# Optimization experiments

Hardware: AMD Instinct MI355X
Metric: run time of the kernel (lower is better)

## Reference

```python
import jax, jax.numpy as jnp
import numpy as np

LN_EPS = 1e-5


def _layer_norm(h, g, b):
    mu = jnp.mean(h, axis=-1, keepdims=True)
    var = jnp.mean((h - mu) ** 2, axis=-1, keepdims=True)
    return (h - mu) / jnp.sqrt(var + LN_EPS) * g + b


def setup_inputs() -> dict:
    key = jax.random.key(0)
    ks = jax.random.split(key, 12)
    B, N, D = 2, 2048, 768
    H, Dh = 12, 64
    Dp = D // 4  # 192, DynamicPositionBias width
    s = lambda fan_in: 1.0 / np.sqrt(fan_in)
    return {
        "x": jax.random.normal(ks[0], (B, N, D), jnp.float32),
        "qkv_w": jax.random.normal(ks[1], (D, 3 * H * Dh), jnp.float32) * s(D),
        "qkv_b": jax.random.normal(ks[2], (3 * H * Dh,), jnp.float32) * 0.02,
        "out_w": jax.random.normal(ks[3], (H * Dh, D), jnp.float32) * s(H * Dh),
        "out_b": jax.random.normal(ks[4], (D,), jnp.float32) * 0.02,
        "dpb_w_in": jax.random.normal(ks[5], (1, Dp), jnp.float32),
        "dpb_b_in": jax.random.normal(ks[6], (Dp,), jnp.float32) * 0.02,
        "dpb_w_hid": jax.random.normal(ks[7], (3, Dp, Dp), jnp.float32) * s(Dp),
        "dpb_b_hid": jax.random.normal(ks[8], (3, Dp), jnp.float32) * 0.02,
        "dpb_ln_g": jnp.ones((4, Dp), jnp.float32),
        "dpb_ln_b": jnp.zeros((4, Dp), jnp.float32),
        "dpb_w_out": jax.random.normal(ks[9], (Dp, 12), jnp.float32) * s(Dp),
        "dpb_b_out": jax.random.normal(ks[10], (12,), jnp.float32) * 0.02,
    }


def _dpb_bias(n, w_in, b_in, w_hid, b_hid, ln_g, ln_b, w_out, b_out):
    # positions -n+1 .. n-1, log-distance transform
    pos = jnp.arange(-n + 1, n, dtype=jnp.float32)[:, None]  # [2n-1, 1]
    pos = jnp.sign(pos) * jnp.log(jnp.abs(pos) + 1.0)
    h = jax.nn.silu(_layer_norm(pos @ w_in + b_in, ln_g[0], ln_b[0]))
    for l in range(3):
        h = jax.nn.silu(_layer_norm(h @ w_hid[l] + b_hid[l], ln_g[l + 1], ln_b[l + 1]))
    vals = h @ w_out + b_out  # [2n-1, H]
    idx = jnp.arange(n)[:, None] - jnp.arange(n)[None, :] + (n - 1)  # [n, n]
    bias = vals[idx]  # [n, n, H]
    return jnp.transpose(bias, (2, 0, 1))  # [H, n, n]


def reference(x, qkv_w, qkv_b, out_w, out_b,
              dpb_w_in, dpb_b_in, dpb_w_hid, dpb_b_hid,
              dpb_ln_g, dpb_ln_b, dpb_w_out, dpb_b_out):
    B, N, D = x.shape
    H = dpb_w_out.shape[-1]
    qkv = x @ qkv_w + qkv_b  # [B, N, 3*H*Dh]
    q, k, v = jnp.split(qkv, 3, axis=-1)
    split_heads = lambda t: jnp.transpose(t.reshape(B, N, H, -1), (0, 2, 1, 3))
    q, k, v = split_heads(q), split_heads(k), split_heads(v)  # [B, H, N, Dh]
    Dh = q.shape[-1]

    bias = _dpb_bias(N, dpb_w_in, dpb_b_in, dpb_w_hid, dpb_b_hid,
                     dpb_ln_g, dpb_ln_b, dpb_w_out, dpb_b_out)  # [H, N, N]

    scale = Dh ** -0.5
    sim = jnp.einsum("bhid,bhjd->bhij", q, k) * scale + bias[None]
    attn = jax.nn.softmax(sim, axis=-1)
    o = jnp.einsum("bhij,bhjd->bhid", attn, v)  # [B, H, N, Dh]
    o = jnp.transpose(o, (0, 2, 1, 3)).reshape(B, N, H * Dh)
    return o @ out_w + out_b
```

## Files before the change

kernel.cpp:

```cpp
#include <hip/hip_runtime.h>
#include <stdint.h>
#include <stddef.h>

typedef __bf16 bf16;
typedef __bf16 bf16x8 __attribute__((ext_vector_type(8)));
typedef float floatx4 __attribute__((ext_vector_type(4)));

typedef __attribute__((address_space(1))) void as1_void;
typedef __attribute__((address_space(3))) void as3_void;

__device__ __forceinline__ void async_ld16(const void* g, void* l) {
    __builtin_amdgcn_global_load_lds((as1_void*)g, (as3_void*)l, 16, 0, 0);
}

__device__ __forceinline__ floatx4 mfma16(bf16x8 a, bf16x8 b, floatx4 c) {
    return __builtin_amdgcn_mfma_f32_16x16x32_bf16(a, b, c, 0, 0, 0);
}

__device__ __forceinline__ unsigned cvtpk_bf16(float lo, float hi) {
    unsigned r;
    asm("v_cvt_pk_bf16_f32 %0, %1, %2" : "=v"(r) : "v"(lo), "v"(hi));
    return r;
}
__device__ __forceinline__ void pl32swap(unsigned &a, unsigned &b) {
    asm("v_permlane32_swap_b32 %0, %1" : "+v"(a), "+v"(b));
}
__device__ __forceinline__ void pl16swap(unsigned &a, unsigned &b) {
    asm("v_permlane16_swap_b32 %0, %1" : "+v"(a), "+v"(b));
}

#define LOG2E 1.4426950408889634f
#define SM_M2 24.0f
#define DP 192

__device__ __forceinline__ float ldsc(const void* p, size_t i, int isbf) {
    return isbf ? (float)((const bf16*)p)[i] : ((const float*)p)[i];
}
__device__ __forceinline__ bf16x8 ld8(const void* p, size_t i, int isbf) {
    if (isbf) return *(const bf16x8*)((const bf16*)p + i);
    const float* f = (const float*)p + i;
    float4 lo = *(const float4*)(f);
    float4 hi = *(const float4*)(f + 4);
    bf16x8 r;
    r[0]=(bf16)lo.x; r[1]=(bf16)lo.y; r[2]=(bf16)lo.z; r[3]=(bf16)lo.w;
    r[4]=(bf16)hi.x; r[5]=(bf16)hi.y; r[6]=(bf16)hi.z; r[7]=(bf16)hi.w;
    return r;
}
__device__ __forceinline__ int get_fl(const uint32_t* lng) {
    return (lng[0] == 0x3F803F80u) ? 1 : 0;
}

__device__ void transpose_body(const void* in, bf16* out, int R, int C,
                               int bx, int by, int fl, bf16 (*tile)[65]) {
    int c0 = bx * 64, r0 = by * 64;
    for (int i = threadIdx.x; i < 64*64; i += 256) {
        int rr = i >> 6, cc = i & 63;
        int gr = r0 + rr, gc = c0 + cc;
        tile[rr][cc] = (gr < R && gc < C)
                       ? (bf16)ldsc(in, (size_t)gr * C + gc, fl) : (bf16)0.0f;
    }
    __syncthreads();
    for (int i = threadIdx.x; i < 64*64; i += 256) {
        int rr = i >> 6, cc = i & 63;
        int oR = c0 + rr, oC = r0 + cc;
        if (oR < C && oC < R) out[(size_t)oR * R + oC] = tile[cc][rr];
    }
}

__global__ __launch_bounds__(256) void prep_kernel(
    const void* __restrict__ qkv_w, const void* __restrict__ out_w,
    bf16* __restrict__ wt_qkv, bf16* __restrict__ wt_out,
    const void* __restrict__ w_hid, const void* __restrict__ w_out,
    bf16* __restrict__ WtH, bf16* __restrict__ Wt12,
    const uint32_t* __restrict__ lngw,
    const void* __restrict__ x, bf16* __restrict__ xbf)
{
    __shared__ bf16 tile[64][65];
    const int fl = get_fl(lngw);
    const int bid = blockIdx.x;
    if (bid < 432) {
        transpose_body(qkv_w, wt_qkv, 768, 2304, bid % 36, bid / 36, fl, tile);
        return;
    }
    if (bid < 576) {
        int b2 = bid - 432;
        transpose_body(out_w, wt_out, 768, 768, b2 % 12, b2 / 12, fl, tile);
        return;
    }
    if (bid < 603) {
        int b2 = bid - 576, l = b2 / 9, t9 = b2 % 9;
        transpose_body((const char*)w_hid + (size_t)l * DP * DP * (fl ? 2 : 4),
                       WtH + (size_t)l * DP * DP, DP, DP, t9 % 3, t9 / 3,
                       fl, tile);
        return;
    }
    if (bid < 606) {
        transpose_body(w_out, Wt12, 192, 12, 0, bid - 603, fl, tile);
        return;
    }
    size_t base = (size_t)(bid - 606) * 6144 + threadIdx.x * 8;
    #pragma unroll
    for (int c = 0; c < 3; c++)
        *(bf16x8*)(xbf + base + c*2048) = ld8(x, base + c*2048, fl);
}

#define GK 768
#define HS 200

__global__ __launch_bounds__(256) void gemm0_dpb_kernel(
    const bf16* __restrict__ A, const bf16* __restrict__ Bt,
    const void* __restrict__ bias, const uint32_t* __restrict__ lngw,
    bf16* __restrict__ out0, bf16* __restrict__ out1, bf16* __restrict__ out2,
    const void* __restrict__ w_in, const void* __restrict__ b_in,
    const void* __restrict__ b_hid, const void* __restrict__ ln_g,
    const void* __restrict__ ln_b, const void* __restrict__ b_out,
    const bf16* __restrict__ WtH, const bf16* __restrict__ Wt12,
    float* __restrict__ vals_t)
{
    __shared__ __align__(16) char smem[16896];
    const int fl = get_fl(lngw);
    const int tid = threadIdx.x;
    const int wave = tid >> 6, lane = tid & 63;
    const int g = lane >> 4, cl = lane & 15;

    if (blockIdx.x >= 576) {
        bf16*  Hb   = (bf16*)smem;
        float* redS = (float*)(smem + 6400);
        float* redQ = (float*)(smem + 6656);
        const int pbase = (blockIdx.x - 576) * 16;

        float tpos[4];
        #pragma unroll
        for (int rg = 0; rg < 4; rg++) {
            int p = pbase + g*4 + rg;
            float pv = (float)p - 2047.0f;
            float sg = (pv > 0.0f) ? 1.0f : ((pv < 0.0f) ? -1.0f : 0.0f);
            tpos[rg] = sg * logf(fabsf(pv) + 1.0f);
        }
        int col[3];
        #pragma unroll
        for (int tt = 0; tt < 3; tt++) col[tt] = (wave*3 + tt)*16 + cl;

        floatx4 acc[3];
        #pragma unroll
        for (int tt = 0; tt < 3; tt++) {
            float wi = ldsc(w_in, col[tt], fl), bi = ldsc(b_in, col[tt], fl);
            #pragma unroll
            for (int rg = 0; rg < 4; rg++) acc[tt][rg] = tpos[rg]*wi + bi;
        }

        #pragma unroll 1
        for (int l = 0; l < 4; l++) {
            float s1[4], s2[4];
            #pragma unroll
            for (int rg = 0; rg < 4; rg++) {
                s1[rg] = acc[0][rg] + acc[1][rg] + acc[2][rg];
                s2[rg] = acc[0][rg]*acc[0][rg] + acc[1][rg]*acc[1][rg]
                       + acc[2][rg]*acc[2][rg];
            }
            #pragma unroll
            for (int m = 1; m <= 8; m <<= 1)
                #pragma unroll
                for (int rg = 0; rg < 4; rg++) {
                    s1[rg] += __shfl_xor(s1[rg], m);
                    s2[rg] += __shfl_xor(s2[rg], m);
                }
            if (cl == 0)
                #pragma unroll
                for (int rg = 0; rg < 4; rg++) {
                    redS[wave*16 + g*4 + rg] = s1[rg];
                    redQ[wave*16 + g*4 + rg] = s2[rg];
                }
            __syncthreads();
            float mu[4], rstd[4];
            #pragma unroll
            for (int rg = 0; rg < 4; rg++) {
                int row = g*4 + rg;
                float S = redS[row] + redS[16+row] + redS[32+row] + redS[48+row];
                float Q = redQ[row] + redQ[16+row] + redQ[32+row] + redQ[48+row];
                float m_ = S * (1.0f/DP);
                float v_ = Q * (1.0f/DP) - m_*m_;
                mu[rg] = m_;
                rstd[rg] = 1.0f / sqrtf(v_ + 1e-5f);
            }
            #pragma unroll
            for (int tt = 0; tt < 3; tt++) {
                float ga = ldsc(ln_g, l*DP + col[tt], fl);
                float be = ldsc(ln_b, l*DP + col[tt], fl);
                #pragma unroll
                for (int rg = 0; rg < 4; rg++) {
                    float y = (acc[tt][rg] - mu[rg]) * rstd[rg] * ga + be;
                    float sil = y / (1.0f + __expf(-y));
                    Hb[(g*4 + rg)*HS + col[tt]] = (bf16)sil;
                }
            }
            __syncthreads();
            if (l == 3) break;
            #pragma unroll
            for (int tt = 0; tt < 3; tt++) {
                float bh = ldsc(b_hid, l*DP + col[tt], fl);
                #pragma unroll
                for (int rg = 0; rg < 4; rg++) acc[tt][rg] = bh;
            }
            const bf16* Wl = WtH + (size_t)l * DP * DP;
            #pragma unroll
            for (int ks = 0; ks < 6; ks++) {
                bf16x8 af = *(const bf16x8*)(Hb + cl*HS + ks*32 + g*8);
                #pragma unroll
                for (int tt = 0; tt < 3; tt++) {
                    bf16x8 bfv = *(const bf16x8*)(Wl + (size_t)col[tt]*DP
                                                  + ks*32 + g*8);
                    acc[tt] = mfma16(af, bfv, acc[tt]);
                }
            }
        }
        if (wave == 0) {
            floatx4 facc = {};
            if (cl < 12) {
                float bo = ldsc(b_out, cl, fl);
                #pragma unroll
                for (int rg = 0; rg < 4; rg++) facc[rg] = bo;
            }
            #pragma unroll
            for (int ks = 0; ks < 6; ks++) {
                bf16x8 af = *(const bf16x8*)(Hb + cl*HS + ks*32 + g*8);
                bf16x8 bfv = {};
                if (cl < 12)
                    bfv = *(const bf16x8*)(Wt12 + (size_t)cl*DP + ks*32 + g*8);
                facc = mfma16(af, bfv, facc);
            }
            if (cl < 12)
                #pragma unroll
                for (int rg = 0; rg < 4; rg++) {
                    int p = pbase + g*4 + rg;
                    if (p < 4095) vals_t[cl*4095 + p] = facc[rg];
                }
        }
        return;
    }

    bf16* As = (bf16*)smem;
    bf16* Bs = (bf16*)(smem + 8192);
    const int xcd8 = blockIdx.x & 7, slot = blockIdx.x >> 3;
    const int m0 = (xcd8*4 + slot/18) * 128, n0 = (slot % 18) * 128;
    const int wm = (wave >> 1) * 64, wn = (wave & 1) * 64;

    const int e0 = wave*512 + lane*8;
    const int e1 = e0 + 2048;
    const int r0 = e0 >> 5, c0e = e0 & 31;
    const int r1 = e1 >> 5, c1e = e1 & 31;
    const bf16* Ag0 = A  + (size_t)(m0 + r0) * GK + c0e;
    const bf16* Ag1 = A  + (size_t)(m0 + r1) * GK + c1e;
    const bf16* Bg0 = Bt + (size_t)(n0 + r0) * GK + c0e;
    const bf16* Bg1 = Bt + (size_t)(n0 + r1) * GK + c1e;
    bf16* Al0 = As + e0;
    bf16* Al1 = As + e1;
    bf16* Bl0 = Bs + e0;
    bf16* Bl1 = Bs + e1;

    const int frow = lane & 15, fk = (lane >> 4) * 8;
    floatx4 acc[4][4] = {};

    for (int k0 = 0; k0 < GK; k0 += 32) {
        __syncthreads();
        async_ld16(Ag0 + k0, Al0);
        async_ld16(Ag1 + k0, Al1);
        async_ld16(Bg0 + k0, Bl0);
        async_ld16(Bg1 + k0, Bl1);
        __syncthreads();
        bf16x8 af[4], bfr[4];
        #pragma unroll
        for (int i = 0; i < 4; i++)
            af[i] = *(const bf16x8*)(As + (wm + i*16 + frow)*32 + fk);
        #pragma unroll
        for (int j = 0; j < 4; j++)
            bfr[j] = *(const bf16x8*)(Bs + (wn + j*16 + frow)*32 + fk);
        #pragma unroll
        for (int i = 0; i < 4; i++)
            #pragma unroll
            for (int j = 0; j < 4; j++)
                acc[i][j] = mfma16(af[i], bfr[j], acc[i][j]);
    }

    #pragma unroll
    for (int i = 0; i < 4; i++) {
        #pragma unroll
        for (int j = 0; j < 4; j++) {
            int Cc = n0 + wn + j*16 + cl;
            float bv = ldsc(bias, Cc, fl);
            #pragma unroll
            for (int rg = 0; rg < 4; rg++) {
                int R = m0 + wm + i*16 + g*4 + rg;
                float val = acc[i][j][rg] + bv;
                int which = Cc / 768;
                int c2 = Cc - which * 768;
                int hh = c2 >> 6, dd = c2 & 63;
                int bb = R >> 11, nn = R & 2047;
                if (which == 2) {
                    out2[(((size_t)(bb*12 + hh) * 64 + dd) * 2048) + nn]
                        = (bf16)val;
                } else {
                    bf16* dst = (which == 0) ? out0 : out1;
                    dst[((size_t)(bb*12 + hh) * 2048 + nn) * 64 + dd] = (bf16)val;
                }
            }
        }
    }
}

__global__ __launch_bounds__(256) void gemm_out(
    const bf16* __restrict__ A, const bf16* __restrict__ Bt,
    const void* __restrict__ bias, const uint32_t* __restrict__ lngw,
    void* __restrict__ out0)
{
    __shared__ __align__(16) bf16 As[128*32];
    __shared__ __align__(16) bf16 Bs[128*32];
    const int fl  = get_fl(lngw);
    const int tid = threadIdx.x;
    const int wave = tid >> 6, lane = tid & 63;
    const int m0 = blockIdx.y * 128, n0 = blockIdx.x * 128;
    const int wm = (wave >> 1) * 64, wn = (wave & 1) * 64;

    const int e0 = wave*512 + lane*8;
    const int e1 = e0 + 2048;
    const int r0 = e0 >> 5, c0e = e0 & 31;
    const int r1 = e1 >> 5, c1e = e1 & 31;
    const bf16* Ag0 = A  + (size_t)(m0 + r0) * GK + c0e;
    const bf16* Ag1 = A  + (size_t)(m0 + r1) * GK + c1e;
    const bf16* Bg0 = Bt + (size_t)(n0 + r0) * GK + c0e;
    const bf16* Bg1 = Bt + (size_t)(n0 + r1) * GK + c1e;
    bf16* Al0 = As + e0;
    bf16* Al1 = As + e1;
    bf16* Bl0 = Bs + e0;
    bf16* Bl1 = Bs + e1;

    const int frow = lane & 15, fk = (lane >> 4) * 8;
    floatx4 acc[4][4] = {};

    for (int k0 = 0; k0 < GK; k0 += 32) {
        __syncthreads();
        async_ld16(Ag0 + k0, Al0);
        async_ld16(Ag1 + k0, Al1);
        async_ld16(Bg0 + k0, Bl0);
        async_ld16(Bg1 + k0, Bl1);
        __syncthreads();
        bf16x8 af[4], bfr[4];
        #pragma unroll
        for (int i = 0; i < 4; i++)
            af[i] = *(const bf16x8*)(As + (wm + i*16 + frow)*32 + fk);
        #pragma unroll
        for (int j = 0; j < 4; j++)
            bfr[j] = *(const bf16x8*)(Bs + (wn + j*16 + frow)*32 + fk);
        #pragma unroll
        for (int i = 0; i < 4; i++)
            #pragma unroll
            for (int j = 0; j < 4; j++)
                acc[i][j] = mfma16(af[i], bfr[j], acc[i][j]);
    }

    const int g = lane >> 4, cl = lane & 15;
    #pragma unroll
    for (int i = 0; i < 4; i++) {
        #pragma unroll
        for (int j = 0; j < 4; j++) {
            int Cc = n0 + wn + j*16 + cl;
            float bv = ldsc(bias, Cc, fl);
            #pragma unroll
            for (int rg = 0; rg < 4; rg++) {
                int R = m0 + wm + i*16 + g*4 + rg;
                float val = acc[i][j][rg] + bv;
                size_t oi = (size_t)R * 768 + Cc;
                if (fl) ((bf16*)out0)[oi]  = (bf16)val;
                else    ((float*)out0)[oi] = val;
            }
        }
    }
}

__global__ __launch_bounds__(256) void attn_kernel(
    const bf16* __restrict__ qws, const bf16* __restrict__ kws,
    const bf16* __restrict__ vwst, const float* __restrict__ vals_t,
    bf16* __restrict__ ows)
{
    __shared__ __align__(16) bf16 Qs[64*72];
    __shared__ __align__(16) bf16 Ks[2][64*72];
    __shared__ __align__(16) bf16 Vt[2][64*72];
    __shared__ float bias_s[2][128];

    const int tid = threadIdx.x;
    const int wave = tid >> 6, lane = tid & 63;
    const int g = lane >> 4, cl = lane & 15;
    const int xcd8 = blockIdx.x & 7, slot = blockIdx.x >> 3;
    const int bh_ = xcd8*3 + (slot >> 5);
    const int q0 = (slot & 31) * 64;
    const int h = bh_ % 12, b = bh_ / 12;
    const size_t bh = (size_t)bh_;
    const bf16* qp  = qws  + bh * 2048 * 64;
    const bf16* kp  = kws  + bh * 2048 * 64;
    const bf16* vpt = vwst + bh * 64 * 2048;
    const float* vrow = vals_t + h * 4095;

    for (int i = tid; i < 512; i += 256) {
        int r = i >> 3, c = (i & 7) * 8;
        *(bf16x8*)(Qs + r*72 + c) = *(const bf16x8*)(qp + (size_t)(q0 + r)*64 + c);
    }

    const int sr0 = tid >> 3, sc0 = (tid & 7) * 8;
    const int sr1 = sr0 + 32;

    bf16x8 kreg0 = *(const bf16x8*)(kp + (size_t)sr0 * 64 + sc0);
    bf16x8 kreg1 = *(const bf16x8*)(kp + (size_t)sr1 * 64 + sc0);
    bf16x8 vreg0 = *(const bf16x8*)(vpt + (size_t)sr0 * 2048 + sc0);
    bf16x8 vreg1 = *(const bf16x8*)(vpt + (size_t)sr1 * 2048 + sc0);
    float  breg  = 0.0f;
    if (tid < 127) breg = vrow[q0 + 1984 + tid];
    *(bf16x8*)(Ks[0] + sr0*72 + sc0) = kreg0;
    *(bf16x8*)(Ks[0] + sr1*72 + sc0) = kreg1;
    *(bf16x8*)(Vt[0] + sr0*72 + sc0) = vreg0;
    *(bf16x8*)(Vt[0] + sr1*72 + sc0) = vreg1;
    if (tid < 127) bias_s[0][tid] = breg * LOG2E - SM_M2;

    kreg0 = *(const bf16x8*)(kp + (size_t)(64 + sr0) * 64 + sc0);
    kreg1 = *(const bf16x8*)(kp + (size_t)(64 + sr1) * 64 + sc0);
    vreg0 = *(const bf16x8*)(vpt + (size_t)sr0 * 2048 + 64 + sc0);
    vreg1 = *(const bf16x8*)(vpt + (size_t)sr1 * 2048 + 64 + sc0);
    if (tid < 127) breg = vrow[q0 - 64 + 1984 + tid];

    __syncthreads();
    bf16x8 aq0 = *(const bf16x8*)(Qs + (wave*16 + cl)*72 + g*8);
    bf16x8 aq1 = *(const bf16x8*)(Qs + (wave*16 + cl)*72 + 32 + g*8);

    floatx4 accO[4] = {};
    float lsum = 0.0f;
    const int il_b = wave*16 + g*4;
    const float c1 = 0.125f * LOG2E;
    const int bbase = wave*16 + cl - 4*g + 63;

    for (int j = 0; j < 32; ++j) {
        const int cur = j & 1;
        if (j + 1 < 32) {
            bf16* Kn = Ks[cur ^ 1];
            bf16* Vn = Vt[cur ^ 1];
            *(bf16x8*)(Kn + sr0*72 + sc0) = kreg0;
            *(bf16x8*)(Kn + sr1*72 + sc0) = kreg1;
            *(bf16x8*)(Vn + sr0*72 + sc0) = vreg0;
            *(bf16x8*)(Vn + sr1*72 + sc0) = vreg1;
            if (tid < 127) bias_s[cur ^ 1][tid] = breg * LOG2E - SM_M2;
        }
        if (j + 2 < 32) {
            const int nj = (j + 2) * 64;
            kreg0 = *(const bf16x8*)(kp + (size_t)(nj + sr0) * 64 + sc0);
            kreg1 = *(const bf16x8*)(kp + (size_t)(nj + sr1) * 64 + sc0);
            vreg0 = *(const bf16x8*)(vpt + (size_t)sr0 * 2048 + nj + sc0);
            vreg1 = *(const bf16x8*)(vpt + (size_t)sr1 * 2048 + nj + sc0);
            if (tid < 127) breg = vrow[q0 - nj + 1984 + tid];
        }

        const bf16* Kc = Ks[cur];
        const bf16* Vc = Vt[cur];
        const float* bs = bias_s[cur];

        floatx4 accS[4];
        #pragma unroll
        for (int jt = 0; jt < 4; jt++) {
            bf16x8 ak0 = *(const bf16x8*)(Kc + (jt*16 + cl)*72 + g*8);
            bf16x8 ak1 = *(const bf16x8*)(Kc + (jt*16 + cl)*72 + 32 + g*8);
            floatx4 z = {};
            z = mfma16(ak0, aq0, z);
            z = mfma16(ak1, aq1, z);
            accS[jt] = z;
        }

        unsigned pk[4][2];
        #pragma unroll
        for (int jt = 0; jt < 4; jt++) {
            float pv[4];
            #pragma unroll
            for (int rg = 0; rg < 4; rg++) {
                float x2 = fmaf(accS[jt][rg], c1, bs[bbase - jt*16 - rg]);
                x2 = fminf(x2, 80.0f);
                pv[rg] = __builtin_amdgcn_exp2f(x2);
            }
            lsum += (pv[0] + pv[1]) + (pv[2] + pv[3]);
            pk[jt][0] = cvtpk_bf16(pv[0], pv[1]);
            pk[jt][1] = cvtpk_bf16(pv[2], pv[3]);
        }

        bf16x8 ap[2];
        #pragma unroll
        for (int kst = 0; kst < 2; kst++) {
            unsigned e0p = pk[2*kst][0], f0p = pk[2*kst+1][0];
            unsigned e1p = pk[2*kst][1], f1p = pk[2*kst+1][1];
            pl32swap(e0p, f0p);
            pl16swap(e0p, f0p);
            pl32swap(e1p, f1p);
            pl16swap(e1p, f1p);
            union { unsigned u[4]; bf16x8 v; } uu;
            uu.u[0] = e0p; uu.u[1] = e1p; uu.u[2] = f0p; uu.u[3] = f1p;
            ap[kst] = uu.v;
        }

        #pragma unroll
        for (int dt = 0; dt < 4; dt++) {
            #pragma unroll
            for (int kst = 0; kst < 2; kst++) {
                bf16x8 bv = *(const bf16x8*)(Vc + (dt*16 + cl)*72 + kst*32 + g*8);
                accO[dt] = mfma16(ap[kst], bv, accO[dt]);
            }
        }

        __syncthreads();
    }

    lsum += __shfl_xor(lsum, 16);
    lsum += __shfl_xor(lsum, 32);

    #pragma unroll
    for (int rg = 0; rg < 4; rg++) {
        float l = __shfl(lsum, g*4 + rg);
        float inv = 1.0f / l;
        size_t row = (size_t)(b*2048 + q0 + il_b + rg) * 768 + h*64;
        #pragma unroll
        for (int dt = 0; dt < 4; dt++)
            ows[row + dt*16 + cl] = (bf16)(accO[dt][rg] * inv);
    }
}

extern "C" void kernel_launch(void* const* d_in, const int* in_sizes, int n_in,
                              void* d_out, int out_size, void* d_ws, size_t ws_size,
                              hipStream_t stream)
{
    (void)in_sizes; (void)n_in; (void)out_size;
    const void* x     = d_in[0];
    const void* qkv_w = d_in[1];
    const void* qkv_b = d_in[2];
    const void* out_w = d_in[3];
    const void* out_b = d_in[4];
    const void* w_in  = d_in[5];
    const void* b_in  = d_in[6];
    const void* w_hid = d_in[7];
    const void* b_hid = d_in[8];
    const void* ln_g  = d_in[9];
    const void* ln_b  = d_in[10];
    const void* w_out = d_in[11];
    const void* b_out = d_in[12];

    const size_t NEED = 4915200 + 4ull*6291456;
    if (ws_size < NEED) return;

    char* ws = (char*)d_ws;
    float* vals_t = (float*)(ws);
    bf16*  wt_qkv = (bf16*)(ws + 196608);
    bf16*  wt_out = (bf16*)(ws + 196608 + 3538944);
    bf16*  q_ws   = (bf16*)(ws + 4915200);
    bf16*  k_ws   = (bf16*)(ws + 4915200 + 6291456);
    bf16*  v_wst  = (bf16*)(ws + 4915200 + 2*6291456);
    bf16*  o_ws   = (bf16*)(ws + 4915200 + 3*6291456);
    bf16*  x_bf   = o_ws;
    bf16*  WtH    = (bf16*)d_out;
    bf16*  Wt12   = WtH + 3*DP*DP;

    prep_kernel<<<1118, 256, 0, stream>>>(qkv_w, out_w, wt_qkv, wt_out,
                                          w_hid, w_out, WtH, Wt12,
                                          (const uint32_t*)ln_g, x, x_bf);
    gemm0_dpb_kernel<<<832, 256, 0, stream>>>(
        x_bf, wt_qkv, qkv_b, (const uint32_t*)ln_g, q_ws, k_ws, v_wst,
        w_in, b_in, b_hid, ln_g, ln_b, b_out, WtH, Wt12, vals_t);
    attn_kernel<<<768, 256, 0, stream>>>(q_ws, k_ws, v_wst, vals_t, o_ws);
    gemm_out<<<dim3(6, 32), 256, 0, stream>>>(o_ws, wt_out, out_b,
                                              (const uint32_t*)ln_g, d_out);
}
```

Baseline: 209.0 us.

## Load V fragments directly to registers in attention, shrink output GEMM tiles

The attention kernel stops staging V through shared memory. Each lane loads its own V MFMA operand fragments from global memory into double-buffered registers one tile ahead, and the shared-memory V buffers go away. A launch-bounds occupancy hint of three blocks per CU is added. The output projection GEMM moves from 128x128 to 64x64 tiles, giving 768 blocks instead of 192 for better CU fill, at the cost of less operand reuse and more register pressure from the V prefetch.

Measured after the change: 249.9 us. 19.6% more time.

```diff
diff --git a/kernel.cpp b/kernel.cpp
--- a/kernel.cpp
+++ b/kernel.cpp
@@ -313,56 +313,48 @@
     const void* __restrict__ bias, const uint32_t* __restrict__ lngw,
     void* __restrict__ out0)
 {
-    __shared__ __align__(16) bf16 As[128*32];
-    __shared__ __align__(16) bf16 Bs[128*32];
+    __shared__ __align__(16) bf16 As[64*32];
+    __shared__ __align__(16) bf16 Bs[64*32];
     const int fl  = get_fl(lngw);
     const int tid = threadIdx.x;
     const int wave = tid >> 6, lane = tid & 63;
-    const int m0 = blockIdx.y * 128, n0 = blockIdx.x * 128;
-    const int wm = (wave >> 1) * 64, wn = (wave & 1) * 64;
-
-    const int e0 = wave*512 + lane*8;
-    const int e1 = e0 + 2048;
+    const int m0 = blockIdx.y * 64, n0 = blockIdx.x * 64;
+    const int wm = (wave >> 1) * 32, wn = (wave & 1) * 32;
+
+    const int e0 = tid * 8;
     const int r0 = e0 >> 5, c0e = e0 & 31;
-    const int r1 = e1 >> 5, c1e = e1 & 31;
     const bf16* Ag0 = A  + (size_t)(m0 + r0) * GK + c0e;
-    const bf16* Ag1 = A  + (size_t)(m0 + r1) * GK + c1e;
     const bf16* Bg0 = Bt + (size_t)(n0 + r0) * GK + c0e;
-    const bf16* Bg1 = Bt + (size_t)(n0 + r1) * GK + c1e;
     bf16* Al0 = As + e0;
-    bf16* Al1 = As + e1;
     bf16* Bl0 = Bs + e0;
-    bf16* Bl1 = Bs + e1;
 
     const int frow = lane & 15, fk = (lane >> 4) * 8;
-    floatx4 acc[4][4] = {};
+    floatx4 acc[2][2] = {};
 
     for (int k0 = 0; k0 < GK; k0 += 32) {
         __syncthreads();
         async_ld16(Ag0 + k0, Al0);
-        async_ld16(Ag1 + k0, Al1);
         async_ld16(Bg0 + k0, Bl0);
-        async_ld16(Bg1 + k0, Bl1);
         __syncthreads();
-        bf16x8 af[4], bfr[4];
-        #pragma unroll
-        for (int i = 0; i < 4; i++)
+        bf16x8 af[2], bfr[2];
+        #pragma unroll
+        for (int i = 0; i < 2; i++)
             af[i] = *(const bf16x8*)(As + (wm + i*16 + frow)*32 + fk);
         #pragma unroll
-        for (int j = 0; j < 4; j++)
+        for (int j = 0; j < 2; j++)
             bfr[j] = *(const bf16x8*)(Bs + (wn + j*16 + frow)*32 + fk);
         #pragma unroll
-        for (int i = 0; i < 4; i++)
-            #pragma unroll
-            for (int j = 0; j < 4; j++)
+        for (int i = 0; i < 2; i++)
+            #pragma unroll
+            for (int j = 0; j < 2; j++)
                 acc[i][j] = mfma16(af[i], bfr[j], acc[i][j]);
     }
 
     const int g = lane >> 4, cl = lane & 15;
     #pragma unroll
-    for (int i = 0; i < 4; i++) {
-        #pragma unroll
-        for (int j = 0; j < 4; j++) {
+    for (int i = 0; i < 2; i++) {
+        #pragma unroll
+        for (int j = 0; j < 2; j++) {
             int Cc = n0 + wn + j*16 + cl;
             float bv = ldsc(bias, Cc, fl);
             #pragma unroll
@@ -377,14 +369,13 @@
     }
 }
 
-__global__ __launch_bounds__(256) void attn_kernel(
+__global__ __launch_bounds__(256, 3) void attn_kernel(
     const bf16* __restrict__ qws, const bf16* __restrict__ kws,
     const bf16* __restrict__ vwst, const float* __restrict__ vals_t,
     bf16* __restrict__ ows)
 {
     __shared__ __align__(16) bf16 Qs[64*72];
     __shared__ __align__(16) bf16 Ks[2][64*72];
-    __shared__ __align__(16) bf16 Vt[2][64*72];
     __shared__ float bias_s[2][128];
 
     const int tid = threadIdx.x;
@@ -410,20 +401,26 @@
 
     bf16x8 kreg0 = *(const bf16x8*)(kp + (size_t)sr0 * 64 + sc0);
     bf16x8 kreg1 = *(const bf16x8*)(kp + (size_t)sr1 * 64 + sc0);
-    bf16x8 vreg0 = *(const bf16x8*)(vpt + (size_t)sr0 * 2048 + sc0);
-    bf16x8 vreg1 = *(const bf16x8*)(vpt + (size_t)sr1 * 2048 + sc0);
     float  breg  = 0.0f;
     if (tid < 127) breg = vrow[q0 + 1984 + tid];
     *(bf16x8*)(Ks[0] + sr0*72 + sc0) = kreg0;
     *(bf16x8*)(Ks[0] + sr1*72 + sc0) = kreg1;
-    *(bf16x8*)(Vt[0] + sr0*72 + sc0) = vreg0;
-    *(bf16x8*)(Vt[0] + sr1*72 + sc0) = vreg1;
     if (tid < 127) bias_s[0][tid] = breg * LOG2E - SM_M2;
+
+    bf16x8 VA[8], VB[8];
+    const bf16* vbase = vpt + (size_t)cl * 2048 + g*8;
+    auto loadV = [&](bf16x8 (&V)[8], int jv) {
+        #pragma unroll
+        for (int dt = 0; dt < 4; dt++)
+            #pragma unroll
+            for (int kst = 0; kst < 2; kst++)
+                V[dt*2 + kst] = *(const bf16x8*)(vbase + (size_t)dt*16*2048
+                                                 + jv + kst*32);
+    };
+    loadV(VA, 0);
 
     kreg0 = *(const bf16x8*)(kp + (size_t)(64 + sr0) * 64 + sc0);
     kreg1 = *(const bf16x8*)(kp + (size_t)(64 + sr1) * 64 + sc0);
-    vreg0 = *(const bf16x8*)(vpt + (size_t)sr0 * 2048 + 64 + sc0);
-    vreg1 = *(const bf16x8*)(vpt + (size_t)sr1 * 2048 + 64 + sc0);
     if (tid < 127) breg = vrow[q0 - 64 + 1984 + tid];
 
     __syncthreads();
@@ -436,28 +433,23 @@
     const float c1 = 0.125f * LOG2E;
     const int bbase = wave*16 + cl - 4*g + 63;
 
-    for (int j = 0; j < 32; ++j) {
+    auto iter = [&](bf16x8 (&VC)[8], bf16x8 (&VN)[8], int j) {
         const int cur = j & 1;
         if (j + 1 < 32) {
             bf16* Kn = Ks[cur ^ 1];
-            bf16* Vn = Vt[cur ^ 1];
             *(bf16x8*)(Kn + sr0*72 + sc0) = kreg0;
             *(bf16x8*)(Kn + sr1*72 + sc0) = kreg1;
-            *(bf16x8*)(Vn + sr0*72 + sc0) = vreg0;
-            *(bf16x8*)(Vn + sr1*72 + sc0) = vreg1;
             if (tid < 127) bias_s[cur ^ 1][tid] = breg * LOG2E - SM_M2;
+            loadV(VN, (j + 1) * 64);
         }
         if (j + 2 < 32) {
             const int nj = (j + 2) * 64;
             kreg0 = *(const bf16x8*)(kp + (size_t)(nj + sr0) * 64 + sc0);
             kreg1 = *(const bf16x8*)(kp + (size_t)(nj + sr1) * 64 + sc0);
-            vreg0 = *(const bf16x8*)(vpt + (size_t)sr0 * 2048 + nj + sc0);
-            vreg1 = *(const bf16x8*)(vpt + (size_t)sr1 * 2048 + nj + sc0);
             if (tid < 127) breg = vrow[q0 - nj + 1984 + tid];
         }
 
         const bf16* Kc = Ks[cur];
-        const bf16* Vc = Vt[cur];
         const float* bs = bias_s[cur];
 
         floatx4 accS[4];
@@ -503,13 +495,16 @@
         #pragma unroll
         for (int dt = 0; dt < 4; dt++) {
             #pragma unroll
-            for (int kst = 0; kst < 2; kst++) {
-                bf16x8 bv = *(const bf16x8*)(Vc + (dt*16 + cl)*72 + kst*32 + g*8);
-                accO[dt] = mfma16(ap[kst], bv, accO[dt]);
-            }
+            for (int kst = 0; kst < 2; kst++)
+                accO[dt] = mfma16(ap[kst], VC[dt*2 + kst], accO[dt]);
         }
 
         __syncthreads();
+    };
+
+    for (int j = 0; j < 32; j += 2) {
+        iter(VA, VB, j);
+        iter(VB, VA, j + 1);
     }
 
     lsum += __shfl_xor(lsum, 16);
@@ -567,6 +562,6 @@
         x_bf, wt_qkv, qkv_b, (const uint32_t*)ln_g, q_ws, k_ws, v_wst,
         w_in, b_in, b_hid, ln_g, ln_b, b_out, WtH, Wt12, vals_t);
     attn_kernel<<<768, 256, 0, stream>>>(q_ws, k_ws, v_wst, vals_t, o_ws);
-    gemm_out<<<dim3(6, 32), 256, 0, stream>>>(o_ws, wt_out, out_b,
-                                              (const uint32_t*)ln_g, d_out);
-}
+    gemm_out<<<dim3(12, 64), 256, 0, stream>>>(o_ws, wt_out, out_b,
+                                               (const uint32_t*)ln_g, d_out);
+}
```

## Double-buffer LDS in QKV and output GEMMs, shrink output GEMM tiles to 64x64

Applied to the files above, without the earlier changes.

Both GEMM main loops now use two LDS stages, issuing the async global-to-LDS load for the next K slice before the MFMAs on the current one, with one barrier per iteration instead of two. This is meant to overlap memory latency with compute. The output projection GEMM also moves from 128x128 to 64x64 tiles, giving 768 blocks instead of 192 to fill the GPU better. In exchange, LDS use grows in the QKV kernel, and the smaller tiles give less data reuse per block.

Measured after the change: 208.9 us. About the same (-0.0%).

```diff
diff --git a/kernel.cpp b/kernel.cpp
--- a/kernel.cpp
+++ b/kernel.cpp
@@ -117,7 +117,7 @@
     const bf16* __restrict__ WtH, const bf16* __restrict__ Wt12,
     float* __restrict__ vals_t)
 {
-    __shared__ __align__(16) char smem[16896];
+    __shared__ __align__(16) char smem[32768];
     const int fl = get_fl(lngw);
     const int tid = threadIdx.x;
     const int wave = tid >> 6, lane = tid & 63;
@@ -239,8 +239,7 @@
         return;
     }
 
-    bf16* As = (bf16*)smem;
-    bf16* Bs = (bf16*)(smem + 8192);
+    bf16* Sb = (bf16*)smem;
     const int xcd8 = blockIdx.x & 7, slot = blockIdx.x >> 3;
     const int m0 = (xcd8*4 + slot/18) * 128, n0 = (slot % 18) * 128;
     const int wm = (wave >> 1) * 64, wn = (wave & 1) * 64;
@@ -253,33 +252,39 @@
     const bf16* Ag1 = A  + (size_t)(m0 + r1) * GK + c1e;
     const bf16* Bg0 = Bt + (size_t)(n0 + r0) * GK + c0e;
     const bf16* Bg1 = Bt + (size_t)(n0 + r1) * GK + c1e;
-    bf16* Al0 = As + e0;
-    bf16* Al1 = As + e1;
-    bf16* Bl0 = Bs + e0;
-    bf16* Bl1 = Bs + e1;
 
     const int frow = lane & 15, fk = (lane >> 4) * 8;
     floatx4 acc[4][4] = {};
 
-    for (int k0 = 0; k0 < GK; k0 += 32) {
-        __syncthreads();
-        async_ld16(Ag0 + k0, Al0);
-        async_ld16(Ag1 + k0, Al1);
-        async_ld16(Bg0 + k0, Bl0);
-        async_ld16(Bg1 + k0, Bl1);
-        __syncthreads();
+    auto stage = [&](int t, int p) {
+        const int k0 = t * 32;
+        bf16* d = Sb + p * 8192;
+        async_ld16(Ag0 + k0, d + e0);
+        async_ld16(Ag1 + k0, d + e1);
+        async_ld16(Bg0 + k0, d + 4096 + e0);
+        async_ld16(Bg1 + k0, d + 4096 + e1);
+    };
+
+    stage(0, 0);
+    __syncthreads();
+    for (int t = 0; t < GK/32; ++t) {
+        const int cur = t & 1;
+        if (t + 1 < GK/32) stage(t + 1, cur ^ 1);
+        const bf16* Ac = Sb + cur*8192;
+        const bf16* Bc = Ac + 4096;
         bf16x8 af[4], bfr[4];
         #pragma unroll
         for (int i = 0; i < 4; i++)
-            af[i] = *(const bf16x8*)(As + (wm + i*16 + frow)*32 + fk);
+            af[i] = *(const bf16x8*)(Ac + (wm + i*16 + frow)*32 + fk);
         #pragma unroll
         for (int j = 0; j < 4; j++)
-            bfr[j] = *(const bf16x8*)(Bs + (wn + j*16 + frow)*32 + fk);
+            bfr[j] = *(const bf16x8*)(Bc + (wn + j*16 + frow)*32 + fk);
         #pragma unroll
         for (int i = 0; i < 4; i++)
             #pragma unroll
             for (int j = 0; j < 4; j++)
                 acc[i][j] = mfma16(af[i], bfr[j], acc[i][j]);
+        __syncthreads();
     }
 
     #pragma unroll
@@ -313,56 +318,54 @@
     const void* __restrict__ bias, const uint32_t* __restrict__ lngw,
     void* __restrict__ out0)
 {
-    __shared__ __align__(16) bf16 As[128*32];
-    __shared__ __align__(16) bf16 Bs[128*32];
+    __shared__ __align__(16) bf16 Sb[2][4096];
     const int fl  = get_fl(lngw);
     const int tid = threadIdx.x;
     const int wave = tid >> 6, lane = tid & 63;
-    const int m0 = blockIdx.y * 128, n0 = blockIdx.x * 128;
-    const int wm = (wave >> 1) * 64, wn = (wave & 1) * 64;
-
-    const int e0 = wave*512 + lane*8;
-    const int e1 = e0 + 2048;
+    const int m0 = blockIdx.y * 64, n0 = blockIdx.x * 64;
+    const int wm = (wave >> 1) * 32, wn = (wave & 1) * 32;
+
+    const int e0 = tid * 8;
     const int r0 = e0 >> 5, c0e = e0 & 31;
-    const int r1 = e1 >> 5, c1e = e1 & 31;
     const bf16* Ag0 = A  + (size_t)(m0 + r0) * GK + c0e;
-    const bf16* Ag1 = A  + (size_t)(m0 + r1) * GK + c1e;
     const bf16* Bg0 = Bt + (size_t)(n0 + r0) * GK + c0e;
-    const bf16* Bg1 = Bt + (size_t)(n0 + r1) * GK + c1e;
-    bf16* Al0 = As + e0;
-    bf16* Al1 = As + e1;
-    bf16* Bl0 = Bs + e0;
-    bf16* Bl1 = Bs + e1;
 
     const int frow = lane & 15, fk = (lane >> 4) * 8;
-    floatx4 acc[4][4] = {};
-
-    for (int k0 = 0; k0 < GK; k0 += 32) {
+    floatx4 acc[2][2] = {};
+
+    auto stage = [&](int t, int p) {
+        const int k0 = t * 32;
+        async_ld16(Ag0 + k0, &Sb[p][e0]);
+        async_ld16(Bg0 + k0, &Sb[p][2048 + e0]);
+    };
+
+    stage(0, 0);
+    __syncthreads();
+    for (int t = 0; t < GK/32; ++t) {
+        const int cur = t & 1;
+        if (t + 1 < GK/32) stage(t + 1, cur ^ 1);
+        const bf16* Ac = Sb[cur];
+        const bf16* Bc = Ac + 2048;
+        bf16x8 af[2], bfr[2];
+        #pragma unroll
+        for (int i = 0; i < 2; i++)
+            af[i] = *(const bf16x8*)(Ac + (wm + i*16 + frow)*32 + fk);
+        #pragma unroll
+        for (int j = 0; j < 2; j++)
+            bfr[j] = *(const bf16x8*)(Bc + (wn + j*16 + frow)*32 + fk);
+        #pragma unroll
+        for (int i = 0; i < 2; i++)
+            #pragma unroll
+            for (int j = 0; j < 2; j++)
+                acc[i][j] = mfma16(af[i], bfr[j], acc[i][j]);
         __syncthreads();
-        async_ld16(Ag0 + k0, Al0);
-        async_ld16(Ag1 + k0, Al1);
-        async_ld16(Bg0 + k0, Bl0);
-        async_ld16(Bg1 + k0, Bl1);
-        __syncthreads();
-        bf16x8 af[4], bfr[4];
-        #pragma unroll
-        for (int i = 0; i < 4; i++)
-            af[i] = *(const bf16x8*)(As + (wm + i*16 + frow)*32 + fk);
-        #pragma unroll
-        for (int j = 0; j < 4; j++)
-            bfr[j] = *(const bf16x8*)(Bs + (wn + j*16 + frow)*32 + fk);
-        #pragma unroll
-        for (int i = 0; i < 4; i++)
-            #pragma unroll
-            for (int j = 0; j < 4; j++)
-                acc[i][j] = mfma16(af[i], bfr[j], acc[i][j]);
     }
 
     const int g = lane >> 4, cl = lane & 15;
     #pragma unroll
-    for (int i = 0; i < 4; i++) {
-        #pragma unroll
-        for (int j = 0; j < 4; j++) {
+    for (int i = 0; i < 2; i++) {
+        #pragma unroll
+        for (int j = 0; j < 2; j++) {
             int Cc = n0 + wn + j*16 + cl;
             float bv = ldsc(bias, Cc, fl);
             #pragma unroll
@@ -567,6 +570,6 @@
         x_bf, wt_qkv, qkv_b, (const uint32_t*)ln_g, q_ws, k_ws, v_wst,
         w_in, b_in, b_hid, ln_g, ln_b, b_out, WtH, Wt12, vals_t);
     attn_kernel<<<768, 256, 0, stream>>>(q_ws, k_ws, v_wst, vals_t, o_ws);
-    gemm_out<<<dim3(6, 32), 256, 0, stream>>>(o_ws, wt_out, out_b,
-                                              (const uint32_t*)ln_g, d_out);
-}
+    gemm_out<<<dim3(12, 64), 256, 0, stream>>>(o_ws, wt_out, out_b,
+                                               (const uint32_t*)ln_g, d_out);
+}
```
